# Performance work log

Measured on AMD Instinct MI355X. Metric: run time of the kernel, lower is better.

The kernel has to match this reference:

```python
import jax, jax.numpy as jnp
import numpy as np

B, T, C = 2, 2048, 2048
H = 16
HS = C // H           # 128
ROT = HS // 2         # 64 partial-rotary dims
BASE = 10000.0


def setup_inputs() -> dict:
    key = jax.random.key(0)
    ks = jax.random.split(key, 9)
    s = 1.0 / np.sqrt(C)
    return {
        "x": jax.random.normal(ks[0], (B, T, C), jnp.float32),
        "Wq": jax.random.normal(ks[1], (C, C), jnp.float32) * s,
        "bq": jax.random.normal(ks[2], (C,), jnp.float32) * 0.02,
        "Wk": jax.random.normal(ks[3], (C, C), jnp.float32) * s,
        "bk": jax.random.normal(ks[4], (C,), jnp.float32) * 0.02,
        "Wv": jax.random.normal(ks[5], (C, C), jnp.float32) * s,
        "bv": jax.random.normal(ks[6], (C,), jnp.float32) * 0.02,
        "Wo": jax.random.normal(ks[7], (C, C), jnp.float32) * s,
        "bo": jax.random.normal(ks[8], (C,), jnp.float32) * 0.02,
    }


def _rotate_half(u):
    u1, u2 = u[..., : u.shape[-1] // 2], u[..., u.shape[-1] // 2 :]
    return jnp.concatenate((-u2, u1), axis=-1)


def _rope_tables(t_len):
    inv_freq = 1.0 / (BASE ** (jnp.arange(0, ROT, 2, dtype=jnp.float32) / ROT))
    freqs = jnp.arange(t_len, dtype=jnp.float32)[:, None] * inv_freq[None, :]
    emb = jnp.concatenate((freqs, freqs), axis=-1)  # [T, ROT]
    return jnp.cos(emb), jnp.sin(emb)


def reference(x, Wq, bq, Wk, bk, Wv, bv, Wo, bo):
    Bs, Ts, Cs = x.shape
    q = (x @ Wq.T + bq).reshape(Bs, Ts, H, HS).transpose(0, 2, 1, 3)  # [B,H,T,HS]
    k = (x @ Wk.T + bk).reshape(Bs, Ts, H, HS).transpose(0, 2, 1, 3)
    v = (x @ Wv.T + bv).reshape(Bs, Ts, H, HS).transpose(0, 2, 1, 3)

    # partial rotary on first ROT dims of each head
    cos, sin = _rope_tables(Ts)  # [T, ROT] broadcast over B,H
    q_rot, q_pass = q[..., :ROT], q[..., ROT:]
    k_rot, k_pass = k[..., :ROT], k[..., ROT:]
    q_rot = q_rot * cos + _rotate_half(q_rot) * sin
    k_rot = k_rot * cos + _rotate_half(k_rot) * sin
    q = jnp.concatenate((q_rot, q_pass), axis=-1)
    k = jnp.concatenate((k_rot, k_pass), axis=-1)

    att = jnp.einsum("bhqd,bhkd->bhqk", q, k) * (1.0 / np.sqrt(HS))
    causal = jnp.tril(jnp.ones((Ts, Ts), dtype=bool))
    att = jnp.where(causal, att, jnp.float32(-jnp.inf))
    att = jax.nn.softmax(att, axis=-1)
    out = jnp.einsum("bhqk,bhkd->bhqd", att, v)          # [B,H,T,HS]
    out = out.transpose(0, 2, 1, 3).reshape(Bs, Ts, Cs)  # [B,T,C]
    return out @ Wo.T + bo
```

## Files before the change

kernel.cpp:

```cpp
#include <hip/hip_runtime.h>
#include <hip/hip_bf16.h>

#define Bdim 2
#define Tdim 2048
#define Cdim 2048
#define Hn   16

using bf16x8 = __attribute__((ext_vector_type(8))) short;
using f32x4  = __attribute__((ext_vector_type(4))) float;
using f32x16 = __attribute__((ext_vector_type(16))) float;
typedef __hip_bfloat16 bf16;

#define VMWAIT(n) asm volatile("s_waitcnt vmcnt(" #n ")" ::: "memory")
#define CROW(r, hi) (((r) & 3) + 8 * ((r) >> 2) + 4 * (hi))
#define QS2 ((float)(0.08838834764831845 * 1.4426950408889634))
#define THR2 11.5415603f

__device__ __forceinline__ void load_lds16(const void* g, void* l) {
  __builtin_amdgcn_global_load_lds(
      (const __attribute__((address_space(1))) void*)g,
      (__attribute__((address_space(3))) void*)l, 16, 0, 0);
}

__device__ __forceinline__ float bf2f(unsigned short u) {
  union { unsigned int i; float f; } x; x.i = ((unsigned int)u) << 16; return x.f;
}
__device__ __forceinline__ unsigned short f2bf(float f) {
  bf16 h = __float2bfloat16(f); return *(unsigned short*)&h;
}
__device__ __forceinline__ unsigned cvtpk(float lo, float hi) {
  unsigned r;
  asm volatile("v_cvt_pk_bf16_f32 %0, %1, %2" : "=v"(r) : "v"(lo), "v"(hi));
  return r;
}

__global__ __launch_bounds__(256) void cvt_all(const float* __restrict__ x,
                                               const float* __restrict__ w0,
                                               const float* __restrict__ w1,
                                               const float* __restrict__ w2,
                                               const float* __restrict__ w3,
                                               bf16* __restrict__ dx,
                                               bf16* __restrict__ d0,
                                               bf16* __restrict__ d1,
                                               bf16* __restrict__ d2,
                                               bf16* __restrict__ d3) {
  const int NX = (Bdim * Tdim * Cdim) / 4;
  const int NW = (Cdim * Cdim) / 4;
  int i = blockIdx.x * 256 + threadIdx.x;
  int stride = gridDim.x * 256;
  for (; i < NX + 4 * NW; i += stride) {
    const float* s; bf16* d; int j;
    if (i < NX) { s = x; d = dx; j = i; }
    else {
      int k = i - NX;
      int wsel = k >> 20;
      j = k & (NW - 1);
      s = wsel == 0 ? w0 : wsel == 1 ? w1 : wsel == 2 ? w2 : w3;
      d = wsel == 0 ? d0 : wsel == 1 ? d1 : wsel == 2 ? d2 : d3;
    }
    float4 v = ((const float4*)s)[j];
    ushort4 o;
    o.x = f2bf(v.x); o.y = f2bf(v.y); o.z = f2bf(v.z); o.w = f2bf(v.w);
    ((ushort4*)d)[j] = o;
  }
}

__global__ __launch_bounds__(256) void rope_tables_k(float2* __restrict__ cst) {
  int idx = blockIdx.x * blockDim.x + threadIdx.x;
  if (idx >= Tdim * 32) return;
  int t = idx >> 5, i = idx & 31;
  double f = pow(10000.0, -(double)i / 32.0);
  double ang = (double)t * f;
  cst[idx] = make_float2((float)cos(ang), (float)sin(ang));
}

__global__ __launch_bounds__(256, 2) void gemmQKV(
    const bf16* __restrict__ A, const bf16* __restrict__ Wcat,
    const float* __restrict__ b0, const float* __restrict__ b1, const float* __restrict__ b2,
    bf16* __restrict__ oq, bf16* __restrict__ ok, bf16* __restrict__ vt,
    const float2* __restrict__ cst) {
  extern __shared__ char lds[];
  const int tid = threadIdx.x, lane = tid & 63, wid = tid >> 6;
  const int l31 = lane & 31, hi = lane >> 5;
  const int wr = wid >> 1, wc = wid & 1;
  const int wbase = wid * 1024;

  const int q8 = gridDim.x >> 3;
  const int swz = ((int)blockIdx.x & 7) * q8 + ((int)blockIdx.x >> 3);
  const int bm = (swz >> 5) * 256;
  const int strip = swz & 31;

  const int rS = tid >> 2, sS = tid & 3;
  const int ssw = (sS ^ ((rS >> 1) & 3)) << 3;
  const bf16* thrA = A + (size_t)(bm + rS) * 2048 + ssw;
  const bf16* thrB = Wcat + (size_t)(strip * 192 + rS) * 2048 + ssw;

#define SA(T, DB) { load_lds16(thrA + (T) * 32, (DB) + wbase);                              \
                    load_lds16(thrA + (size_t)64 * 2048 + (T) * 32, (DB) + 4096 + wbase);   \
                    load_lds16(thrA + (size_t)128 * 2048 + (T) * 32, (DB) + 8192 + wbase);  \
                    load_lds16(thrA + (size_t)192 * 2048 + (T) * 32, (DB) + 12288 + wbase); }
#define SB(T, DB) { load_lds16(thrB + (T) * 32, (DB) + 16384 + wbase);                      \
                    load_lds16(thrB + (size_t)64 * 2048 + (T) * 32, (DB) + 20480 + wbase);  \
                    load_lds16(thrB + (size_t)128 * 2048 + (T) * 32, (DB) + 24576 + wbase); }

  f32x16 acc[4][3] = {};
  bf16x8 afr[4], bfr[3];
  const int q2 = (l31 >> 1) & 3;
  const int aoff = (wr * 128 + l31) * 64;
  const int boff = 16384 + (wc * 96 + l31) * 64;
  const int sl0 = (hi ^ q2) << 4;
  const int sl1 = sl0 ^ 32;

#define READF(PB, SL)                                                        \
  {                                                                          \
    const char* _p = (PB);                                                   \
    _Pragma("unroll")                                                        \
    for (int m_ = 0; m_ < 4; ++m_)                                           \
      afr[m_] = *(const bf16x8*)(_p + aoff + m_ * 2048 + (SL));              \
    _Pragma("unroll")                                                        \
    for (int n_ = 0; n_ < 3; ++n_)                                           \
      bfr[n_] = *(const bf16x8*)(_p + boff + n_ * 2048 + (SL));              \
  }

#define MF12()                                                               \
  __builtin_amdgcn_s_setprio(1);                                             \
  _Pragma("unroll")                                                          \
  for (int m_ = 0; m_ < 4; ++m_)                                             \
    _Pragma("unroll")                                                        \
    for (int n_ = 0; n_ < 3; ++n_)                                           \
      acc[m_][n_] = __builtin_amdgcn_mfma_f32_32x32x16_bf16(                 \
          afr[m_], bfr[n_], acc[m_][n_], 0, 0, 0);                           \
  __builtin_amdgcn_s_setprio(0);

  SA(0, lds); SB(0, lds);
  VMWAIT(0);
  __builtin_amdgcn_s_barrier();
  __builtin_amdgcn_sched_barrier(0);
  READF(lds, sl0);

  const int NT = 64;
  for (int t = 0; t < NT; ++t) {
    char* bufC = lds + (t & 1) * 28672;
    char* bufO = lds + ((t + 1) & 1) * 28672;
    if (t + 1 < NT) { SA(t + 1, bufO); SB(t + 1, bufO); }
    MF12();
    READF(bufC, sl1);
    MF12();
    if (t + 1 < NT) {
      VMWAIT(0);
      __builtin_amdgcn_s_barrier();
      __builtin_amdgcn_sched_barrier(0);
      READF(bufO, sl0);
    }
  }

  __syncthreads();
  if (wc == 1 && (strip & 1)) {
    const int col0 = strip * 192 + 96;
    const int mat = col0 >> 11;
    if (mat < 2) {
      const int oc0 = col0 & 2047;
      const float bv = (mat == 0 ? b0 : b1)[oc0 + l31];
      #pragma unroll
      for (int m = 0; m < 4; ++m)
        #pragma unroll
        for (int g = 0; g < 4; ++g) {
          f32x4 v;
          v[0] = acc[m][0][4 * g + 0] + bv;
          v[1] = acc[m][0][4 * g + 1] + bv;
          v[2] = acc[m][0][4 * g + 2] + bv;
          v[3] = acc[m][0][4 * g + 3] + bv;
          *(f32x4*)(lds + (((((wr * 4 + m) * 4 + g) * 2 + hi) * 32) + l31) * 16) = v;
        }
    }
  }
  __syncthreads();

  #pragma unroll
  for (int m = 0; m < 4; ++m) {
    const int rowb = bm + wr * 128 + m * 32;
    const int bb = rowb >> 11, tb = rowb & 2047;
    #pragma unroll
    for (int n = 0; n < 3; ++n) {
      const int col0 = strip * 192 + wc * 96 + n * 32;
      const int mat = col0 >> 11;
      const int oc0 = col0 & 2047;
      const float bv = (mat == 0 ? b0 : mat == 1 ? b1 : b2)[oc0 + l31];
      if (mat == 2) {
        const int hh = oc0 >> 7;
        bf16* dst = vt + ((size_t)((bb * 16 + hh) * 128 + (oc0 & 127) + l31)) * 2048 + tb;
        #pragma unroll
        for (int g = 0; g < 4; ++g) {
          ushort4 pk;
          pk.x = f2bf(acc[m][n][4 * g + 0] + bv);
          pk.y = f2bf(acc[m][n][4 * g + 1] + bv);
          pk.z = f2bf(acc[m][n][4 * g + 2] + bv);
          pk.w = f2bf(acc[m][n][4 * g + 3] + bv);
          *(ushort4*)(dst + g * 8 + hi * 4) = pk;
        }
      } else {
        const float qs = (mat == 0) ? QS2 : 1.0f;
        bf16* obf = (mat == 0) ? oq : ok;
        const float* bp = (mat == 0) ? b0 : b1;
        const int hb = (col0 >> 5) & 3;
        if (hb == 0) {
          if (n == 2) {
            #pragma unroll
            for (int g = 0; g < 4; ++g) {
              f32x4 ux = *(const f32x4*)(lds + (((((wr * 4 + m) * 4 + g) * 2 + hi) * 32) + l31) * 16);
              #pragma unroll
              for (int j = 0; j < 4; ++j) {
                const int r = 4 * g + j;
                const int row = rowb + j + 8 * g + 4 * hi;
                const int tt = row & 2047;
                float2 cs = cst[tt * 32 + l31];
                float u0 = acc[m][n][r] + bv;
                float u1 = ux[j];
                obf[(size_t)row * 2048 + oc0 + l31] =
                    __float2bfloat16((u0 * cs.x - u1 * cs.y) * qs);
                obf[(size_t)row * 2048 + oc0 + 32 + l31] =
                    __float2bfloat16((u1 * cs.x + u0 * cs.y) * qs);
              }
            }
          } else {
            const float bv1 = bp[oc0 + 32 + l31];
            #pragma unroll
            for (int r = 0; r < 16; ++r) {
              const int row = rowb + (r & 3) + 8 * (r >> 2) + 4 * hi;
              const int tt = row & 2047;
              float2 cs = cst[tt * 32 + l31];
              float u0 = acc[m][n][r] + bv;
              float u1 = acc[m][n + 1][r] + bv1;
              obf[(size_t)row * 2048 + oc0 + l31] =
                  __float2bfloat16((u0 * cs.x - u1 * cs.y) * qs);
              obf[(size_t)row * 2048 + oc0 + 32 + l31] =
                  __float2bfloat16((u1 * cs.x + u0 * cs.y) * qs);
            }
          }
        } else if (hb >= 2) {
          #pragma unroll
          for (int r = 0; r < 16; ++r) {
            const int row = rowb + (r & 3) + 8 * (r >> 2) + 4 * hi;
            obf[(size_t)row * 2048 + oc0 + l31] =
                __float2bfloat16((acc[m][n][r] + bv) * qs);
          }
        }
      }
    }
  }
#undef SA
#undef SB
#undef READF
#undef MF12
}

__global__ __launch_bounds__(512, 2) void gemmWo(
    const bf16* __restrict__ A, const bf16* __restrict__ W0,
    const float* __restrict__ b0, float* __restrict__ out, int K, int nby) {
  extern __shared__ char lds[];
  const int tid = threadIdx.x, lane = tid & 63, wid = tid >> 6;
  const int l15 = lane & 15, lhi = lane >> 4;
  const int wr = wid >> 2, wc = wid & 3;
  const int fb = (wc & 1) | ((wc >> 1) << 2);

  const int q8 = gridDim.x >> 3;
  const int swz = ((int)blockIdx.x & 7) * q8 + ((int)blockIdx.x >> 3);
  const int bm = (swz / nby) * 128, bn = (swz % nby) * 256;
  const bf16* Asrc = A + (size_t)bm * K;
  const bf16* Wsrc = W0 + (size_t)bn * K;

  const bf16 *sA0, *sA1, *sB00, *sB01, *sB10, *sB11;
  {
    int c = tid, r = c >> 3, sl = c & 7;
    size_t off = (size_t)r * K + ((sl ^ (r & 7)) << 3);
    sA0 = Asrc + off;
    sA1 = Asrc + (size_t)64 * K + off;
    sB00 = Wsrc + off;
    sB10 = Wsrc + (size_t)128 * K + off;
  }
  {
    int c = 512 + tid, r = c >> 3, sl = c & 7;
    size_t off = (size_t)r * K + ((sl ^ (r & 7)) << 3);
    sB01 = Wsrc + off;
    sB11 = Wsrc + (size_t)128 * K + off;
  }
  const int ldsA = wid * 1024;

#define SA0(t) load_lds16(sA0 + (t) * 64, lds + ((t) & 1) * 49152 + ldsA)
#define SA1(t) load_lds16(sA1 + (t) * 64, lds + ((t) & 1) * 49152 + 8192 + ldsA)
#define SB0(t) { load_lds16(sB00 + (t) * 64, lds + ((t) & 1) * 49152 + 16384 + ldsA); \
                 load_lds16(sB01 + (t) * 64, lds + ((t) & 1) * 49152 + 24576 + ldsA); }
#define SB1(t) { load_lds16(sB10 + (t) * 64, lds + ((t) & 1) * 49152 + 32768 + ldsA); \
                 load_lds16(sB11 + (t) * 64, lds + ((t) & 1) * 49152 + 40960 + ldsA); }

  f32x4 acc[4][4] = {};
  const int NT = K / 64;
  const int NI = NT / 2;
  const int asw = (l15 & 7) << 4;
  bf16x8 afr[2][2], bfr0[2][2], bfr1[2][2];

#define READ_A(BASE)                                                            \
  _Pragma("unroll")                                                             \
  for (int ii = 0; ii < 2; ++ii)                                                \
    _Pragma("unroll")                                                           \
    for (int kk = 0; kk < 2; ++kk)                                              \
      afr[ii][kk] = *(const bf16x8*)((BASE) + (wr * 32 + ii * 16 + l15) * 128   \
                                     + ((kk * 64 + lhi * 16) ^ asw));

#define READ_B(BASE, DST)                                                       \
  _Pragma("unroll")                                                             \
  for (int j = 0; j < 2; ++j)                                                   \
    _Pragma("unroll")                                                           \
    for (int kk = 0; kk < 2; ++kk)                                              \
      DST[j][kk] = *(const bf16x8*)((BASE) + ((fb + 2 * j) * 16 + l15) * 128    \
                                    + ((kk * 64 + lhi * 16) ^ asw));

#define MFMA_Q(MH, NH, BF)                                                      \
  __builtin_amdgcn_s_setprio(1);                                                \
  _Pragma("unroll")                                                             \
  for (int ii = 0; ii < 2; ++ii)                                                \
    _Pragma("unroll")                                                           \
    for (int j = 0; j < 2; ++j)                                                 \
      _Pragma("unroll")                                                         \
      for (int kk = 0; kk < 2; ++kk)                                            \
        acc[(MH) * 2 + ii][(NH) * 2 + j] =                                      \
            __builtin_amdgcn_mfma_f32_16x16x32_bf16(                            \
                afr[ii][kk], BF[j][kk], acc[(MH) * 2 + ii][(NH) * 2 + j], 0, 0, 0); \
  __builtin_amdgcn_s_setprio(0);

#define BAR_IN()                                                                \
  __builtin_amdgcn_s_barrier();                                                 \
  asm volatile("s_waitcnt lgkmcnt(0)" ::: "memory");                            \
  __builtin_amdgcn_sched_barrier(0);

#define BAR_OUT() __builtin_amdgcn_s_barrier();

  SA0(0); SB0(0); SB1(0); SA1(0);
  SA0(1); SB0(1); SB1(1);
  VMWAIT(5);
  __builtin_amdgcn_s_barrier();

  char* const buf0 = lds;
  char* const buf1 = lds + 49152;

  for (int i = 0; i < NI; ++i) {
    const int t0 = 2 * i, t1 = t0 + 1;
    const bool lastI = (i == NI - 1);

    READ_A(buf0);
    READ_B(buf0 + 16384, bfr0);
    SA1(t1);
    BAR_IN(); MFMA_Q(0, 0, bfr0); BAR_OUT();

    READ_B(buf0 + 32768, bfr1);
    if (!lastI) SA0(t0 + 2);
    BAR_IN(); MFMA_Q(0, 1, bfr1); BAR_OUT();

    READ_A(buf0 + 8192);
    if (!lastI) SB0(t0 + 2);
    BAR_IN(); MFMA_Q(1, 0, bfr0); BAR_OUT();

    if (!lastI) { SB1(t0 + 2); VMWAIT(5); } else VMWAIT(0);
    BAR_IN(); MFMA_Q(1, 1, bfr1); BAR_OUT();

    READ_A(buf1);
    READ_B(buf1 + 16384, bfr0);
    if (!lastI) SA1(t0 + 2);
    BAR_IN(); MFMA_Q(0, 0, bfr0); BAR_OUT();

    READ_B(buf1 + 32768, bfr1);
    if (!lastI) SA0(t1 + 2);
    BAR_IN(); MFMA_Q(0, 1, bfr1); BAR_OUT();

    READ_A(buf1 + 8192);
    if (!lastI) SB0(t1 + 2);
    BAR_IN(); MFMA_Q(1, 0, bfr0); BAR_OUT();

    if (!lastI) { SB1(t1 + 2); VMWAIT(5); }
    BAR_IN(); MFMA_Q(1, 1, bfr1); BAR_OUT();
  }

  #pragma unroll
  for (int mi = 0; mi < 4; ++mi) {
    const int row = bm + (mi >> 1) * 64 + wr * 32 + (mi & 1) * 16 + lhi * 4;
    #pragma unroll
    for (int nj = 0; nj < 4; ++nj) {
      const int col = bn + (nj >> 1) * 128 + (fb + 2 * (nj & 1)) * 16 + l15;
      const float bv = b0[col];
      #pragma unroll
      for (int r = 0; r < 4; ++r)
        out[(size_t)(row + r) * 2048 + col] = acc[mi][nj][r] + bv;
    }
  }
#undef SA0
#undef SA1
#undef SB0
#undef SB1
#undef READ_A
#undef READ_B
#undef MFMA_Q
#undef BAR_IN
#undef BAR_OUT
}

__global__ __launch_bounds__(256, 2) void attn_kernel(const bf16* __restrict__ Q,
                                                      const bf16* __restrict__ Kb,
                                                      const bf16* __restrict__ Vt,
                                                      bf16* __restrict__ O) {
  extern __shared__ char lds[];
  const int tid = threadIdx.x, lane = tid & 63, wave = tid >> 6;
  const int l31 = lane & 31, hi = lane >> 5;
  const int hi16 = hi << 4;

  const int bid = blockIdx.x;
  const int half = bid >> 8;
  const int idx = bid & 255;
  const int g = idx >> 5;
  const int qt = half ? g : (15 - g);
  const int bh = idx & 31;
  const int b = bh >> 4, h = bh & 15;
  const size_t bT = (size_t)b * Tdim;

  const int qb = qt * 128 + wave * 32;
  const int myq = qb + l31;

  bf16x8 qf[8];
  {
    const bf16* qrow = Q + (bT + myq) * Cdim + h * 128;
    #pragma unroll
    for (int ds = 0; ds < 8; ++ds)
      qf[ds] = *(const bf16x8*)(qrow + ds * 16 + hi * 8);
  }

  auto stageKV = [&](int kt) {
    const int k0 = kt * 64;
    char* kb = lds + (kt & 1) * 16384;
    char* vb = lds + 32768 + (kt & 1) * 16384;
    #pragma unroll
    for (int i = 0; i < 4; ++i) {
      int cb = i * 256 + wave * 64;
      int c = cb + lane;
      {
        int row = c >> 4, slot = c & 15;
        load_lds16(Kb + (bT + k0 + row) * Cdim + h * 128 + ((slot ^ (row & 7)) << 3),
                   kb + cb * 16);
      }
      {
        int row = c >> 3, slot = c & 7;
        load_lds16(Vt + ((size_t)(bh * 128 + row)) * Tdim + k0 + ((slot ^ (row & 7)) << 3),
                   vb + cb * 16);
      }
    }
  };

  f32x16 o[4] = {};
  float mrun = -1e30f, lrun = 0.f;

  const int nt = 2 * (qt + 1);
  stageKV(0);

  for (int kt = 0; kt < nt; ++kt) {
    if (kt + 1 < nt) { stageKV(kt + 1); VMWAIT(8); } else { VMWAIT(0); }
    __syncthreads();
    const char* kbuf = lds + (kt & 1) * 16384;
    const char* vbuf = lds + 32768 + (kt & 1) * 16384;
    const int k0 = kt * 64;

    const bool active = (k0 <= qb + 31);
    if (active) {
      f32x16 s0 = {}, s1 = {};
      const int krow0 = l31, krow1 = 32 + l31;
      const int ksw = (l31 & 7) << 4;
      __builtin_amdgcn_s_setprio(1);
      #pragma unroll
      for (int ds = 0; ds < 8; ++ds) {
        const int boff = (ds * 32 + hi16) ^ ksw;
        bf16x8 kf0 = *(const bf16x8*)(kbuf + krow0 * 256 + boff);
        bf16x8 kf1 = *(const bf16x8*)(kbuf + krow1 * 256 + boff);
        s0 = __builtin_amdgcn_mfma_f32_32x32x16_bf16(kf0, qf[ds], s0, 0, 0, 0);
        s1 = __builtin_amdgcn_mfma_f32_32x32x16_bf16(kf1, qf[ds], s1, 0, 0, 0);
      }
      __builtin_amdgcn_s_setprio(0);

      if (k0 + 63 > qb) {
        #pragma unroll
        for (int r = 0; r < 16; ++r) {
          const int key = k0 + CROW(r, hi);
          if (key > myq)      s0[r] = -1e30f;
          if (key + 32 > myq) s1[r] = -1e30f;
        }
      }

      float tm[16];
      #pragma unroll
      for (int r = 0; r < 16; ++r) tm[r] = fmaxf(s0[r], s1[r]);
      #pragma unroll
      for (int st = 8; st > 0; st >>= 1)
        #pragma unroll
        for (int r = 0; r < st; ++r) tm[r] = fmaxf(tm[r], tm[r + st]);
      float mx = fmaxf(tm[0], __shfl_xor(tm[0], 32));

      if (!__all(mx <= mrun + THR2)) {
        const float mnew = fmaxf(mrun, mx);
        const float scl = __builtin_amdgcn_exp2f(mrun - mnew);
        lrun *= scl;
        #pragma unroll
        for (int r = 0; r < 16; ++r) {
          const float sr = __shfl(scl, CROW(r, hi));
          o[0][r] *= sr; o[1][r] *= sr; o[2][r] *= sr; o[3][r] *= sr;
        }
        mrun = mnew;
      }

      float p0[16], p1[16], sp[16];
      #pragma unroll
      for (int r = 0; r < 16; ++r) {
        p0[r] = __builtin_amdgcn_exp2f(s0[r] - mrun);
        p1[r] = __builtin_amdgcn_exp2f(s1[r] - mrun);
        sp[r] = p0[r] + p1[r];
      }
      #pragma unroll
      for (int st = 8; st > 0; st >>= 1)
        #pragma unroll
        for (int r = 0; r < st; ++r) sp[r] += sp[r + st];
      float ps = sp[0] + __shfl_xor(sp[0], 32);
      lrun += ps;

      unsigned u0[8], u1[8];
      #pragma unroll
      for (int gg = 0; gg < 4; ++gg) {
        u0[gg * 2 + 0] = cvtpk(p0[gg * 4 + 0], p0[gg * 4 + 1]);
        u0[gg * 2 + 1] = cvtpk(p0[gg * 4 + 2], p0[gg * 4 + 3]);
        u1[gg * 2 + 0] = cvtpk(p1[gg * 4 + 0], p1[gg * 4 + 1]);
        u1[gg * 2 + 1] = cvtpk(p1[gg * 4 + 2], p1[gg * 4 + 3]);
      }
      bf16x8 paf[4];
      #pragma unroll
      for (int s = 0; s < 2; ++s) {
        const unsigned* us = s ? u1 : u0;
        #pragma unroll
        for (int gp = 0; gp < 2; ++gp) {
          unsigned snd0 = hi ? us[4 * gp + 0] : us[4 * gp + 2];
          unsigned snd1 = hi ? us[4 * gp + 1] : us[4 * gp + 3];
          unsigned rcv0 = __shfl_xor((int)snd0, 32);
          unsigned rcv1 = __shfl_xor((int)snd1, 32);
          union { unsigned w[4]; bf16x8 v; } fr;
          if (hi == 0) {
            fr.w[0] = us[4 * gp + 0]; fr.w[1] = us[4 * gp + 1];
            fr.w[2] = rcv0;           fr.w[3] = rcv1;
          } else {
            fr.w[0] = rcv0;           fr.w[1] = rcv1;
            fr.w[2] = us[4 * gp + 2]; fr.w[3] = us[4 * gp + 3];
          }
          paf[s * 2 + gp] = fr.v;
        }
      }

      __builtin_amdgcn_s_setprio(1);
      #pragma unroll
      for (int dblk = 0; dblk < 4; ++dblk) {
        const int d = dblk * 32 + l31;
        const int vswz = (d & 7) << 4;
        #pragma unroll
        for (int ks = 0; ks < 4; ++ks) {
          bf16x8 vf = *(const bf16x8*)(vbuf + d * 128 + ((ks * 32 + hi16) ^ vswz));
          o[dblk] = __builtin_amdgcn_mfma_f32_32x32x16_bf16(paf[ks], vf, o[dblk], 0, 0, 0);
        }
      }
      __builtin_amdgcn_s_setprio(0);
    }
    __syncthreads();
  }

  const float inv = 1.f / lrun;
  #pragma unroll
  for (int r = 0; r < 16; ++r) {
    const float ir = __shfl(inv, CROW(r, hi));
    const int qrow = qb + CROW(r, hi);
    bf16* orow = O + (bT + qrow) * Cdim + h * 128;
    #pragma unroll
    for (int dblk = 0; dblk < 4; ++dblk)
      orow[dblk * 32 + l31] = __float2bfloat16(o[dblk][r] * ir);
  }
}

extern "C" void kernel_launch(void* const* d_in, const int* in_sizes, int n_in,
                              void* d_out, int out_size, void* d_ws, size_t ws_size,
                              hipStream_t stream) {
  const float* x  = (const float*)d_in[0];
  const float* Wq = (const float*)d_in[1];
  const float* bq = (const float*)d_in[2];
  const float* Wk = (const float*)d_in[3];
  const float* bk = (const float*)d_in[4];
  const float* Wv = (const float*)d_in[5];
  const float* bv = (const float*)d_in[6];
  const float* Wo = (const float*)d_in[7];
  const float* bo = (const float*)d_in[8];

  char* ws = (char*)d_ws;
  const size_t SZ_X  = (size_t)Bdim * Tdim * Cdim * 2;
  const size_t SZ_W  = (size_t)Cdim * Cdim * 2;
  bf16* x_bf  = (bf16*)(ws);
  bf16* Wq_bf = (bf16*)(ws + SZ_X);
  bf16* Wk_bf = (bf16*)(ws + SZ_X + SZ_W);
  bf16* Wv_bf = (bf16*)(ws + SZ_X + 2 * SZ_W);
  bf16* Wo_bf = (bf16*)(ws + SZ_X + 3 * SZ_W);
  bf16* q_bf  = (bf16*)(ws + SZ_X + 4 * SZ_W);
  bf16* k_bf  = (bf16*)(ws + 2 * SZ_X + 4 * SZ_W);
  bf16* v_t   = (bf16*)(ws + 3 * SZ_X + 4 * SZ_W);
  bf16* a_bf  = (bf16*)(ws + 4 * SZ_X + 4 * SZ_W);
  float2* cst = (float2*)(ws + 5 * SZ_X + 4 * SZ_W);

  const int K = Cdim;

  rope_tables_k<<<(Tdim * 32 + 255) / 256, 256, 0, stream>>>(cst);
  cvt_all<<<2048, 256, 0, stream>>>(x, Wq, Wk, Wv, Wo,
                                    x_bf, Wq_bf, Wk_bf, Wv_bf, Wo_bf);

  gemmQKV<<<512, 256, 57344, stream>>>(
      x_bf, Wq_bf, bq, bk, bv, q_bf, k_bf, v_t, cst);

  attn_kernel<<<512, 256, 65536, stream>>>(q_bf, k_bf, v_t, a_bf);

  gemmWo<<<256, 512, 98304, stream>>>(
      a_bf, Wo_bf, bo, (float*)d_out, K, 8);
}
```

Baseline: 237.0 us.

## Retile QKV GEMM to 256x128 head-aligned tiles and fuse rope table into convert

```diff
diff --git a/kernel.cpp b/kernel.cpp
--- a/kernel.cpp
+++ b/kernel.cpp
@@ -34,20 +34,31 @@
   return r;
 }
 
-__global__ __launch_bounds__(256) void cvt_all(const float* __restrict__ x,
-                                               const float* __restrict__ w0,
-                                               const float* __restrict__ w1,
-                                               const float* __restrict__ w2,
-                                               const float* __restrict__ w3,
-                                               bf16* __restrict__ dx,
-                                               bf16* __restrict__ d0,
-                                               bf16* __restrict__ d1,
-                                               bf16* __restrict__ d2,
-                                               bf16* __restrict__ d3) {
+__global__ __launch_bounds__(256) void cvt_rope(const float* __restrict__ x,
+                                                const float* __restrict__ w0,
+                                                const float* __restrict__ w1,
+                                                const float* __restrict__ w2,
+                                                const float* __restrict__ w3,
+                                                bf16* __restrict__ dx,
+                                                bf16* __restrict__ d0,
+                                                bf16* __restrict__ d1,
+                                                bf16* __restrict__ d2,
+                                                bf16* __restrict__ d3,
+                                                float2* __restrict__ cst) {
+  if (blockIdx.x >= 2048) {
+    int idx = ((int)blockIdx.x - 2048) * 256 + threadIdx.x;
+    if (idx < Tdim * 32) {
+      int t = idx >> 5, i = idx & 31;
+      double f = pow(10000.0, -(double)i / 32.0);
+      double ang = (double)t * f;
+      cst[idx] = make_float2((float)cos(ang), (float)sin(ang));
+    }
+    return;
+  }
   const int NX = (Bdim * Tdim * Cdim) / 4;
   const int NW = (Cdim * Cdim) / 4;
   int i = blockIdx.x * 256 + threadIdx.x;
-  int stride = gridDim.x * 256;
+  const int stride = 2048 * 256;
   for (; i < NX + 4 * NW; i += stride) {
     const float* s; bf16* d; int j;
     if (i < NX) { s = x; d = dx; j = i; }
@@ -65,16 +76,7 @@
   }
 }
 
-__global__ __launch_bounds__(256) void rope_tables_k(float2* __restrict__ cst) {
-  int idx = blockIdx.x * blockDim.x + threadIdx.x;
-  if (idx >= Tdim * 32) return;
-  int t = idx >> 5, i = idx & 31;
-  double f = pow(10000.0, -(double)i / 32.0);
-  double ang = (double)t * f;
-  cst[idx] = make_float2((float)cos(ang), (float)sin(ang));
-}
-
-__global__ __launch_bounds__(256, 2) void gemmQKV(
+__global__ __launch_bounds__(256, 3) void gemmQKV(
     const bf16* __restrict__ A, const bf16* __restrict__ Wcat,
     const float* __restrict__ b0, const float* __restrict__ b1, const float* __restrict__ b2,
     bf16* __restrict__ oq, bf16* __restrict__ ok, bf16* __restrict__ vt,
@@ -87,27 +89,26 @@
 
   const int q8 = gridDim.x >> 3;
   const int swz = ((int)blockIdx.x & 7) * q8 + ((int)blockIdx.x >> 3);
-  const int bm = (swz >> 5) * 256;
-  const int strip = swz & 31;
+  const int bm = (swz / 48) * 256;
+  const int strip = swz % 48;
 
   const int rS = tid >> 2, sS = tid & 3;
   const int ssw = (sS ^ ((rS >> 1) & 3)) << 3;
   const bf16* thrA = A + (size_t)(bm + rS) * 2048 + ssw;
-  const bf16* thrB = Wcat + (size_t)(strip * 192 + rS) * 2048 + ssw;
+  const bf16* thrB = Wcat + (size_t)(strip * 128 + rS) * 2048 + ssw;
 
 #define SA(T, DB) { load_lds16(thrA + (T) * 32, (DB) + wbase);                              \
                     load_lds16(thrA + (size_t)64 * 2048 + (T) * 32, (DB) + 4096 + wbase);   \
                     load_lds16(thrA + (size_t)128 * 2048 + (T) * 32, (DB) + 8192 + wbase);  \
                     load_lds16(thrA + (size_t)192 * 2048 + (T) * 32, (DB) + 12288 + wbase); }
 #define SB(T, DB) { load_lds16(thrB + (T) * 32, (DB) + 16384 + wbase);                      \
-                    load_lds16(thrB + (size_t)64 * 2048 + (T) * 32, (DB) + 20480 + wbase);  \
-                    load_lds16(thrB + (size_t)128 * 2048 + (T) * 32, (DB) + 24576 + wbase); }
-
-  f32x16 acc[4][3] = {};
-  bf16x8 afr[4], bfr[3];
+                    load_lds16(thrB + (size_t)64 * 2048 + (T) * 32, (DB) + 20480 + wbase); }
+
+  f32x16 acc[4][2] = {};
+  bf16x8 afr[4], bfr[2];
   const int q2 = (l31 >> 1) & 3;
   const int aoff = (wr * 128 + l31) * 64;
-  const int boff = 16384 + (wc * 96 + l31) * 64;
+  const int boff = 16384 + (wc * 64 + l31) * 64;
   const int sl0 = (hi ^ q2) << 4;
   const int sl1 = sl0 ^ 32;
 
@@ -118,16 +119,16 @@
     for (int m_ = 0; m_ < 4; ++m_)                                           \
       afr[m_] = *(const bf16x8*)(_p + aoff + m_ * 2048 + (SL));              \
     _Pragma("unroll")                                                        \
-    for (int n_ = 0; n_ < 3; ++n_)                                           \
+    for (int n_ = 0; n_ < 2; ++n_)                                           \
       bfr[n_] = *(const bf16x8*)(_p + boff + n_ * 2048 + (SL));              \
   }
 
-#define MF12()                                                               \
+#define MF8()                                                                \
   __builtin_amdgcn_s_setprio(1);                                             \
   _Pragma("unroll")                                                          \
   for (int m_ = 0; m_ < 4; ++m_)                                             \
     _Pragma("unroll")                                                        \
-    for (int n_ = 0; n_ < 3; ++n_)                                           \
+    for (int n_ = 0; n_ < 2; ++n_)                                           \
       acc[m_][n_] = __builtin_amdgcn_mfma_f32_32x32x16_bf16(                 \
           afr[m_], bfr[n_], acc[m_][n_], 0, 0, 0);                           \
   __builtin_amdgcn_s_setprio(0);
@@ -140,12 +141,12 @@
 
   const int NT = 64;
   for (int t = 0; t < NT; ++t) {
-    char* bufC = lds + (t & 1) * 28672;
-    char* bufO = lds + ((t + 1) & 1) * 28672;
+    char* bufC = lds + (t & 1) * 24576;
+    char* bufO = lds + ((t + 1) & 1) * 24576;
     if (t + 1 < NT) { SA(t + 1, bufO); SB(t + 1, bufO); }
-    MF12();
+    MF8();
     READF(bufC, sl1);
-    MF12();
+    MF8();
     if (t + 1 < NT) {
       VMWAIT(0);
       __builtin_amdgcn_s_barrier();
@@ -154,39 +155,16 @@
     }
   }
 
-  __syncthreads();
-  if (wc == 1 && (strip & 1)) {
-    const int col0 = strip * 192 + 96;
-    const int mat = col0 >> 11;
-    if (mat < 2) {
-      const int oc0 = col0 & 2047;
-      const float bv = (mat == 0 ? b0 : b1)[oc0 + l31];
-      #pragma unroll
-      for (int m = 0; m < 4; ++m)
-        #pragma unroll
-        for (int g = 0; g < 4; ++g) {
-          f32x4 v;
-          v[0] = acc[m][0][4 * g + 0] + bv;
-          v[1] = acc[m][0][4 * g + 1] + bv;
-          v[2] = acc[m][0][4 * g + 2] + bv;
-          v[3] = acc[m][0][4 * g + 3] + bv;
-          *(f32x4*)(lds + (((((wr * 4 + m) * 4 + g) * 2 + hi) * 32) + l31) * 16) = v;
-        }
-    }
-  }
-  __syncthreads();
-
+  const int mat = strip >> 4;
   #pragma unroll
   for (int m = 0; m < 4; ++m) {
     const int rowb = bm + wr * 128 + m * 32;
     const int bb = rowb >> 11, tb = rowb & 2047;
-    #pragma unroll
-    for (int n = 0; n < 3; ++n) {
-      const int col0 = strip * 192 + wc * 96 + n * 32;
-      const int mat = col0 >> 11;
-      const int oc0 = col0 & 2047;
-      const float bv = (mat == 0 ? b0 : mat == 1 ? b1 : b2)[oc0 + l31];
-      if (mat == 2) {
+    if (mat == 2) {
+      #pragma unroll
+      for (int n = 0; n < 2; ++n) {
+        const int oc0 = ((strip & 15) * 128 + wc * 64 + n * 32) & 2047;
+        const float bv = b2[oc0 + l31];
         const int hh = oc0 >> 7;
         bf16* dst = vt + ((size_t)((bb * 16 + hh) * 128 + (oc0 & 127) + l31)) * 2048 + tb;
         #pragma unroll
@@ -198,50 +176,34 @@
           pk.w = f2bf(acc[m][n][4 * g + 3] + bv);
           *(ushort4*)(dst + g * 8 + hi * 4) = pk;
         }
+      }
+    } else {
+      const float qs = (mat == 0) ? QS2 : 1.0f;
+      bf16* obf = (mat == 0) ? oq : ok;
+      const float* bp = (mat == 0) ? b0 : b1;
+      const int oc0 = (strip & 15) * 128 + wc * 64;
+      if (wc == 0) {
+        const float bl = bp[oc0 + l31], bh2 = bp[oc0 + 32 + l31];
+        #pragma unroll
+        for (int r = 0; r < 16; ++r) {
+          const int row = rowb + (r & 3) + 8 * (r >> 2) + 4 * hi;
+          const int tt = row & 2047;
+          float2 cs = cst[tt * 32 + l31];
+          float u0 = acc[m][0][r] + bl;
+          float u1 = acc[m][1][r] + bh2;
+          obf[(size_t)row * 2048 + oc0 + l31] =
+              __float2bfloat16((u0 * cs.x - u1 * cs.y) * qs);
+          obf[(size_t)row * 2048 + oc0 + 32 + l31] =
+              __float2bfloat16((u1 * cs.x + u0 * cs.y) * qs);
+        }
       } else {
-        const float qs = (mat == 0) ? QS2 : 1.0f;
-        bf16* obf = (mat == 0) ? oq : ok;
-        const float* bp = (mat == 0) ? b0 : b1;
-        const int hb = (col0 >> 5) & 3;
-        if (hb == 0) {
-          if (n == 2) {
-            #pragma unroll
-            for (int g = 0; g < 4; ++g) {
-              f32x4 ux = *(const f32x4*)(lds + (((((wr * 4 + m) * 4 + g) * 2 + hi) * 32) + l31) * 16);
-              #pragma unroll
-              for (int j = 0; j < 4; ++j) {
-                const int r = 4 * g + j;
-                const int row = rowb + j + 8 * g + 4 * hi;
-                const int tt = row & 2047;
-                float2 cs = cst[tt * 32 + l31];
-                float u0 = acc[m][n][r] + bv;
-                float u1 = ux[j];
-                obf[(size_t)row * 2048 + oc0 + l31] =
-                    __float2bfloat16((u0 * cs.x - u1 * cs.y) * qs);
-                obf[(size_t)row * 2048 + oc0 + 32 + l31] =
-                    __float2bfloat16((u1 * cs.x + u0 * cs.y) * qs);
-              }
-            }
-          } else {
-            const float bv1 = bp[oc0 + 32 + l31];
-            #pragma unroll
-            for (int r = 0; r < 16; ++r) {
-              const int row = rowb + (r & 3) + 8 * (r >> 2) + 4 * hi;
-              const int tt = row & 2047;
-              float2 cs = cst[tt * 32 + l31];
-              float u0 = acc[m][n][r] + bv;
-              float u1 = acc[m][n + 1][r] + bv1;
-              obf[(size_t)row * 2048 + oc0 + l31] =
-                  __float2bfloat16((u0 * cs.x - u1 * cs.y) * qs);
-              obf[(size_t)row * 2048 + oc0 + 32 + l31] =
-                  __float2bfloat16((u1 * cs.x + u0 * cs.y) * qs);
-            }
-          }
-        } else if (hb >= 2) {
+        #pragma unroll
+        for (int n = 0; n < 2; ++n) {
+          const float bv = bp[oc0 + n * 32 + l31];
           #pragma unroll
           for (int r = 0; r < 16; ++r) {
             const int row = rowb + (r & 3) + 8 * (r >> 2) + 4 * hi;
-            obf[(size_t)row * 2048 + oc0 + l31] =
+            obf[(size_t)row * 2048 + oc0 + n * 32 + l31] =
                 __float2bfloat16((acc[m][n][r] + bv) * qs);
           }
         }
@@ -251,7 +213,7 @@
 #undef SA
 #undef SB
 #undef READF
-#undef MF12
+#undef MF8
 }
 
 __global__ __launch_bounds__(512, 2) void gemmWo(
@@ -613,11 +575,10 @@
 
   const int K = Cdim;
 
-  rope_tables_k<<<(Tdim * 32 + 255) / 256, 256, 0, stream>>>(cst);
-  cvt_all<<<2048, 256, 0, stream>>>(x, Wq, Wk, Wv, Wo,
-                                    x_bf, Wq_bf, Wk_bf, Wv_bf, Wo_bf);
-
-  gemmQKV<<<512, 256, 57344, stream>>>(
+  cvt_rope<<<2304, 256, 0, stream>>>(x, Wq, Wk, Wv, Wo,
+                                     x_bf, Wq_bf, Wk_bf, Wv_bf, Wo_bf, cst);
+
+  gemmQKV<<<768, 256, 49152, stream>>>(
       x_bf, Wq_bf, bq, bk, bv, q_bf, k_bf, v_t, cst);
 
   attn_kernel<<<512, 256, 65536, stream>>>(q_bf, k_bf, v_t, a_bf);
```

Result: slower. 249.9 us (+5.5%).
